# Performance work log

Measured on AMD Instinct MI355X. Metric: run time of the kernel, lower is better.

## Reference

```python
import jax, jax.numpy as jnp
import numpy as np

RANK = 8
ALPHA = 16.0
SCALING = ALPHA / RANK


def setup_inputs() -> dict:
    key = jax.random.key(0)
    ks = jax.random.split(key, 13)
    T, B, D = 8, 1024, 1024
    H1, H2, H3 = 2048, 2048, 1024
    r = RANK
    def n(k, shape, scale):
        return jax.random.normal(k, shape, dtype=jnp.float32) * scale
    return {
        "x": n(ks[0], (T, B, D), 1.0),
        "k0": n(ks[1], (D, H1), D ** -0.5),
        "b0": n(ks[2], (H1,), 0.02),
        "d0": n(ks[3], (D, r, T), D ** -0.5),
        "u0": n(ks[4], (r, H1, T), 0.02),  # zeros-init in original; random for nontrivial test
        "k1": n(ks[5], (H1, H2), H1 ** -0.5),
        "b1": n(ks[6], (H2,), 0.02),
        "d1": n(ks[7], (H1, r, T), H1 ** -0.5),
        "u1": n(ks[8], (r, H2, T), 0.02),
        "k2": n(ks[9], (H2, H3), H2 ** -0.5),
        "b2": n(ks[10], (H3,), 0.02),
        "d2": n(ks[11], (H2, r, T), H2 ** -0.5),
        "u2": n(ks[12], (r, H3, T), 0.02),
    }


def _lora_dense(h, k, b, d, u):
    # frozen base matmul: [t,b,i] @ [i,f] -> [t,b,f]
    base = jnp.einsum('tbi,if->tbf', h, k) + b
    # per-task low-rank adapter: down [i,r,t], up [r,f,t]
    delta = jnp.einsum('tbi,irt,rft->tbf', h, d, u) * SCALING
    return base + delta


def reference(x, k0, b0, d0, u0, k1, b1, d1, u1, k2, b2, d2, u2):
    h = jax.nn.relu(_lora_dense(x, k0, b0, d0, u0))
    h = jax.nn.relu(_lora_dense(h, k1, b1, d1, u1))
    h = _lora_dense(h, k2, b2, d2, u2)  # no activation on final layer
    return h
```

## Files before the change

### kernel.cpp

```cpp
#include <hip/hip_runtime.h>

typedef unsigned short u16;
typedef __attribute__((ext_vector_type(8))) __bf16 bf16x8;
typedef __attribute__((ext_vector_type(8))) unsigned short u16x8;
typedef __attribute__((ext_vector_type(4))) unsigned short u16x4;
typedef __attribute__((ext_vector_type(4))) float f32x4;

__device__ __forceinline__ float bf2f(u16 h) {
    return __uint_as_float(((unsigned int)h) << 16);
}
__device__ __forceinline__ u16 f2bf(float f) {
    unsigned int u = __float_as_uint(f);
    u += 0x7fffu + ((u >> 16) & 1u);
    return (u16)(u >> 16);
}
__device__ __forceinline__ bf16x8 zero_bf16x8() {
    union { unsigned int u[4]; bf16x8 v; } z;
    z.u[0] = z.u[1] = z.u[2] = z.u[3] = 0u;
    return z.v;
}
__device__ __forceinline__ void gload_lds16(const void* g, void* l) {
    __builtin_amdgcn_global_load_lds(
        (const __attribute__((address_space(1))) unsigned int*)g,
        (__attribute__((address_space(3))) unsigned int*)l, 16, 0, 0);
}
__device__ __forceinline__ void store_out(u16* p, float v)  { *p = f2bf(v); }
__device__ __forceinline__ void store_out(float* p, float v){ *p = v; }


__device__ __forceinline__ void do_cvt(
    const float* __restrict__ in, u16* __restrict__ out, int blk)
{
    int i = (blk * 256 + (int)threadIdx.x) * 8;
    float4 a = *(const float4*)(in + i);
    float4 b = *(const float4*)(in + i + 4);
    u16x8 o;
    o[0] = f2bf(a.x); o[1] = f2bf(a.y); o[2] = f2bf(a.z); o[3] = f2bf(a.w);
    o[4] = f2bf(b.x); o[5] = f2bf(b.y); o[6] = f2bf(b.z); o[7] = f2bf(b.w);
    *(u16x8*)(out + i) = o;
}

__device__ __forceinline__ void do_transpose64(
    const float* __restrict__ in, u16* __restrict__ out, int K, int F, int t)
{
    __shared__ u16 tt[64][68];
    int fb = t % (F >> 6), kb = t / (F >> 6);
    int f0 = fb << 6, k0 = kb << 6;
    int c  = threadIdx.x & 15;
    int r  = threadIdx.x >> 4;
#pragma unroll
    for (int p = 0; p < 4; ++p) {
        int row = p * 16 + r;
        float4 v = *(const float4*)(in + (size_t)(k0 + row) * F + f0 + c * 4);
        u16x4 w;
        w[0] = f2bf(v.x); w[1] = f2bf(v.y); w[2] = f2bf(v.z); w[3] = f2bf(v.w);
        *(u16x4*)&tt[row][c * 4] = w;
    }
    __syncthreads();
#pragma unroll
    for (int p = 0; p < 4; ++p) {
        int f = p * 16 + r;
        u16x4 w;
        w[0] = tt[c * 4 + 0][f];
        w[1] = tt[c * 4 + 1][f];
        w[2] = tt[c * 4 + 2][f];
        w[3] = tt[c * 4 + 3][f];
        *(u16x4*)(out + (size_t)(f0 + f) * K + k0 + c * 4) = w;
    }
}

__device__ __forceinline__ void do_prep_d(
    const float* __restrict__ d, u16* __restrict__ o, int K, int blk)
{
    int i = blk * 256 + (int)threadIdx.x;
    int r = i & 7;
    int k = (i >> 3) % K;
    int t = i / (K * 8);
    o[i] = f2bf(d[((size_t)k * 8 + r) * 8 + t]);
}

__device__ __forceinline__ void do_prep_u(
    const float* __restrict__ u, u16* __restrict__ o, int F, int blk)
{
    int i = blk * 256 + (int)threadIdx.x;
    int r = i & 7;
    int f = (i >> 3) % F;
    int t = i / (F * 8);
    o[i] = f2bf(u[((size_t)r * F + f) * 8 + t] * 2.0f);
}

__global__ __launch_bounds__(256) void prep_all(
    const float* x, const float* k0, const float* k1, const float* k2,
    const float* d0, const float* d1, const float* d2,
    const float* u0, const float* u1, const float* u2,
    u16* xb, u16* k0T, u16* k1T, u16* k2T,
    u16* dS0, u16* dS1, u16* dS2, u16* uS0, u16* uS1, u16* uS2)
{
    int b = blockIdx.x;
    if      (b < 4096) do_cvt(x, xb, b);
    else if (b < 4608) do_transpose64(k0, k0T, 1024, 2048, b - 4096);
    else if (b < 5632) do_transpose64(k1, k1T, 2048, 2048, b - 4608);
    else if (b < 6144) do_transpose64(k2, k2T, 2048, 1024, b - 5632);
    else if (b < 6400) do_prep_d(d0, dS0, 1024, b - 6144);
    else if (b < 6912) do_prep_d(d1, dS1, 2048, b - 6400);
    else if (b < 7424) do_prep_d(d2, dS2, 2048, b - 6912);
    else if (b < 7936) do_prep_u(u0, uS0, 2048, b - 7424);
    else if (b < 8448) do_prep_u(u1, uS1, 2048, b - 7936);
    else               do_prep_u(u2, uS2, 1024, b - 8448);
}

__global__ __launch_bounds__(256) void lora_down(
    const u16* __restrict__ H, const u16* __restrict__ dS,
    u16* __restrict__ Aout, int K)
{
    int gt   = blockIdx.x * 256 + threadIdx.x;
    int row  = gt >> 3;
    int oct  = gt & 7;
    int task = row >> 10;
    const u16* hrow = H  + (size_t)row * K;
    const u16* dt   = dS + (size_t)task * K * 8;
    float acc[8];
#pragma unroll
    for (int r = 0; r < 8; ++r) acc[r] = 0.f;
    int kpt  = K >> 3;
    int kbeg = oct * kpt;
    for (int kk = kbeg; kk < kbeg + kpt; kk += 8) {
        u16x8 h8 = *(const u16x8*)(hrow + kk);
#pragma unroll
        for (int j = 0; j < 8; ++j) {
            float hv = bf2f(h8[j]);
            u16x8 dv = *(const u16x8*)(dt + (size_t)(kk + j) * 8);
#pragma unroll
            for (int r = 0; r < 8; ++r)
                acc[r] += hv * bf2f(dv[r]);
        }
    }
#pragma unroll
    for (int r = 0; r < 8; ++r) {
        acc[r] += __shfl_xor(acc[r], 1);
        acc[r] += __shfl_xor(acc[r], 2);
        acc[r] += __shfl_xor(acc[r], 4);
    }
    if (oct == 0) {
        u16x8 o;
#pragma unroll
        for (int r = 0; r < 8; ++r) o[r] = f2bf(acc[r]);
        *(u16x8*)(Aout + (size_t)row * 8) = o;
    }
}


#define WVMC do { if constexpr (SAL + SBL == 4) { \
                    asm volatile("s_waitcnt vmcnt(4)" ::: "memory"); \
                  } else if constexpr (SAL + SBL == 3) { \
                    asm volatile("s_waitcnt vmcnt(3)" ::: "memory"); \
                  } else { \
                    asm volatile("s_waitcnt vmcnt(2)" ::: "memory"); } } while (0)
#define WVMP do { if constexpr (SAL == 2) { \
                    asm volatile("s_waitcnt vmcnt(2)" ::: "memory"); \
                  } else { \
                    asm volatile("s_waitcnt vmcnt(1)" ::: "memory"); } } while (0)
#define WVM0  asm volatile("s_waitcnt vmcnt(0)" ::: "memory")
#define PHASE_END do { __builtin_amdgcn_sched_barrier(0); \
                       __builtin_amdgcn_s_barrier(); } while (0)

#define DS_A(c, mh) do { \
    _Pragma("unroll") for (int mm = 0; mm < NMH; ++mm) \
    _Pragma("unroll") for (int ks = 0; ks < 2; ++ks) \
        aF[mm][ks] = *(const bf16x8*)((const char*)&sA[c][0] + \
                       arowb + ((mh)*NMH+mm)*4096 + (ks ? cb1 : cb0)); } while (0)

#define DS_B(c, nh, bset) do { \
    _Pragma("unroll") for (int nn = 0; nn < NBH; ++nn) \
    _Pragma("unroll") for (int ks = 0; ks < 2; ++ks) \
        bset[nn][ks] = *(const bf16x8*)((const char*)&sB[c][0] + \
                       browb + ((nh)*NBH+nn)*8192 + (ks ? cb1 : cb0)); } while (0)

#define MFMAQ(mh, nh, bset) do { \
    _Pragma("unroll") for (int ks = 0; ks < 2; ++ks) \
    _Pragma("unroll") for (int mm = 0; mm < NMH; ++mm) \
    _Pragma("unroll") for (int nn = 0; nn < NBH; ++nn) \
        acc[(mh)*NMH+mm][(nh)*NBH+nn] = __builtin_amdgcn_mfma_f32_16x16x32_bf16( \
            aF[mm][ks], bset[nn][ks], acc[(mh)*NMH+mm][(nh)*NBH+nn], 0, 0, 0); } while (0)

#define STAGE_A(c, h, kt) do { \
    _Pragma("unroll") for (int s = 0; s < SAL; ++s) \
        gload_lds16((const char*)A + (size_t)(unsigned)(aBase + \
                      ((h)*BMH + s*64)*(K*2) + (kt)*128), \
                    (char*)&sA[c][0] + (h)*(BMH*128) + s*8192 + tdst); } while (0)

#define STAGE_B(c, h, kt) do { \
    _Pragma("unroll") for (int s = 0; s < SBL; ++s) \
        gload_lds16((const char*)BT + (size_t)(unsigned)(bBase + \
                      ((h)*BNH + s*64)*(K*2) + (kt)*128), \
                    (char*)&sB[c][0] + (h)*(BNH*128) + s*8192 + tdst); } while (0)

template<int RELU, int BM, int BN, int WPEU, typename OUT_T>
__global__ __launch_bounds__(512, WPEU) void gemm_lora8(
    const u16* __restrict__ A, const u16* __restrict__ BT,
    const u16* __restrict__ ALR, const u16* __restrict__ US,
    const float* __restrict__ bias, OUT_T* __restrict__ C,
    int N, int K)
{
    constexpr int SAL = BM / 128;
    constexpr int SBL = BN / 128;
    constexpr int NMH = BM / 64;
    constexpr int NMB = BM / 32;
    constexpr int NBH = BN / 128;
    constexpr int NBN = BN / 64;
    constexpr int BMH = BM / 2;
    constexpr int BNH = BN / 2;

    __shared__ __align__(16) u16 sA[2][BM * 64];
    __shared__ __align__(16) u16 sB[2][BN * 64];

    const int tid  = threadIdx.x;
    const int lane = tid & 63;
    const int wave = tid >> 6;
    const int wr   = wave >> 2;
    const int wc   = wave & 3;
    const int l15  = lane & 15;
    const int lg   = lane >> 4;

    const int nwg = gridDim.x;
    const int orig = blockIdx.x;
    const int q = nwg >> 3, r = nwg & 7;
    const int x = orig & 7, o = orig >> 3;
    const int wg = (x < r ? x * (q + 1) : r * (q + 1) + (x - r) * q) + o;
    const int nbn  = N / BN;
    const int bm   = wg / nbn;
    const int bn   = wg % nbn;
    const int brow = bm * BM;
    const int bcol = bn * BN;
    const int task = brow >> 10;

    const int trow = tid >> 3;
    const int tkc  = (tid & 7) ^ (trow & 7);
    const int tdst = tid * 16;
    const int aBase = (brow + trow) * (K * 2) + tkc * 16;
    const int bBase = (bcol + trow) * (K * 2) + tkc * 16;

    const int rp    = l15 & 7;
    const int cb0   = ((lg ^ (rp & 3)) << 4) | ((rp & 4) << 4);
    const int cb1   = cb0 ^ 64;
    const int arowb = (wr * 16 + l15) * 128;
    const int browb = (wc * 16 + l15) * 128;

    f32x4 acc[NMB][NBN];
    const f32x4 zf = {0.f, 0.f, 0.f, 0.f};
#pragma unroll
    for (int m = 0; m < NMB; ++m)
#pragma unroll
        for (int n = 0; n < NBN; ++n) acc[m][n] = zf;

    bf16x8 aF[NMH][2], bF0[NBH][2], bF1[NBH][2];

    STAGE_A(0, 0, 0); STAGE_B(0, 0, 0); STAGE_A(0, 1, 0); STAGE_B(0, 1, 0);
    STAGE_A(1, 0, 1); STAGE_B(1, 0, 1);
    WVMC;
    PHASE_END;
    DS_A(0, 0); DS_B(0, 0, bF0);

    const int iters = K >> 7;
#pragma unroll 1
    for (int i = 0; i < iters; ++i) {
        const int t1 = 2 * i + 1, t2 = 2 * i + 2, t3 = 2 * i + 3;
        const bool nl = (i + 1 < iters);

        STAGE_A(1, 1, t1);
        MFMAQ(0, 0, bF0);
        DS_B(0, 1, bF1);
        PHASE_END;
        STAGE_B(1, 1, t1);
        MFMAQ(0, 1, bF1);
        DS_A(0, 1);
        PHASE_END;
        if (nl) STAGE_A(0, 0, t2);
        MFMAQ(1, 0, bF0);
        if (nl) { WVMP; } else { WVM0; }
        PHASE_END;
        if (nl) STAGE_B(0, 0, t2);
        MFMAQ(1, 1, bF1);
        DS_A(1, 0); DS_B(1, 0, bF0);
        PHASE_END;
        if (nl) STAGE_A(0, 1, t2);
        MFMAQ(0, 0, bF0);
        DS_B(1, 1, bF1);
        PHASE_END;
        if (nl) STAGE_B(0, 1, t2);
        MFMAQ(0, 1, bF1);
        DS_A(1, 1);
        PHASE_END;
        if (nl) STAGE_A(1, 0, t3);
        MFMAQ(1, 0, bF0);
        if (nl) { WVMP; }
        PHASE_END;
        if (nl) STAGE_B(1, 0, t3);
        MFMAQ(1, 1, bF1);
        if (nl) { DS_A(0, 0); DS_B(0, 0, bF0); }
        PHASE_END;
    }

    bf16x8 z8 = zero_bf16x8();
    bf16x8 bU[NBN];
#pragma unroll
    for (int n = 0; n < NBN; ++n) {
        int col = bcol + n * 64 + wc * 16 + l15;
        bU[n] = (lg == 0) ? *(const bf16x8*)(US + ((size_t)task * N + col) * 8) : z8;
    }
#pragma unroll
    for (int m = 0; m < NMB; ++m) {
        int row = brow + m * 32 + wr * 16 + l15;
        bf16x8 aL = (lg == 0) ? *(const bf16x8*)(ALR + (size_t)row * 8) : z8;
#pragma unroll
        for (int n = 0; n < NBN; ++n)
            acc[m][n] = __builtin_amdgcn_mfma_f32_16x16x32_bf16(
                aL, bU[n], acc[m][n], 0, 0, 0);
    }

#pragma unroll
    for (int n = 0; n < NBN; ++n) {
        int col  = bcol + n * 64 + wc * 16 + l15;
        float bv = bias[col];
#pragma unroll
        for (int m = 0; m < NMB; ++m) {
            int row0 = brow + m * 32 + wr * 16 + lg * 4;
#pragma unroll
            for (int rr = 0; rr < 4; ++rr) {
                float v = acc[m][n][rr] + bv;
                if (RELU) v = fmaxf(v, 0.0f);
                store_out(&C[(size_t)(row0 + rr) * N + col], v);
            }
        }
    }
}


extern "C" void kernel_launch(void* const* d_in, const int* in_sizes, int n_in,
                              void* d_out, int out_size, void* d_ws, size_t ws_size,
                              hipStream_t stream) {
    const float* x  = (const float*)d_in[0];
    const float* k0 = (const float*)d_in[1];
    const float* b0 = (const float*)d_in[2];
    const float* d0 = (const float*)d_in[3];
    const float* u0 = (const float*)d_in[4];
    const float* k1 = (const float*)d_in[5];
    const float* b1 = (const float*)d_in[6];
    const float* d1 = (const float*)d_in[7];
    const float* u1 = (const float*)d_in[8];
    const float* k2 = (const float*)d_in[9];
    const float* b2 = (const float*)d_in[10];
    const float* d2 = (const float*)d_in[11];
    const float* u2 = (const float*)d_in[12];

    const int T = 8, B = 1024, D = 1024, H1 = 2048, H2 = 2048, H3 = 1024;
    const int M = T * B;

    u16* w = (u16*)d_ws;
    size_t off = 0;
    u16* xb  = w + off; off += (size_t)M * D;
    u16* k0T = w + off; off += (size_t)H1 * D;
    u16* k1T = w + off; off += (size_t)H2 * H1;
    u16* k2T = w + off; off += (size_t)H3 * H2;
    u16* dS0 = w + off; off += (size_t)T * D * 8;
    u16* dS1 = w + off; off += (size_t)T * H1 * 8;
    u16* dS2 = w + off; off += (size_t)T * H2 * 8;
    u16* uS0 = w + off; off += (size_t)T * H1 * 8;
    u16* uS1 = w + off; off += (size_t)T * H2 * 8;
    u16* uS2 = w + off; off += (size_t)T * H3 * 8;
    u16* h1  = w + off; off += (size_t)M * H1;
    u16* h2  = w + off; off += (size_t)M * H2;
    u16* Ab  = w + off; off += (size_t)M * 8;
    (void)ws_size; (void)in_sizes; (void)n_in; (void)out_size;

    prep_all<<<8704, 256, 0, stream>>>(
        x, k0, k1, k2, d0, d1, d2, u0, u1, u2,
        xb, k0T, k1T, k2T, dS0, dS1, dS2, uS0, uS1, uS2);

    lora_down<<<(M * 8) / 256, 256, 0, stream>>>(xb, dS0, Ab, D);
    gemm_lora8<1, 256, 256, 2, u16><<<(M / 256) * (H1 / 256), 512, 0, stream>>>(
        xb, k0T, Ab, uS0, b0, h1, H1, D);
    lora_down<<<(M * 8) / 256, 256, 0, stream>>>(h1, dS1, Ab, H1);
    gemm_lora8<1, 256, 256, 2, u16><<<(M / 256) * (H2 / 256), 512, 0, stream>>>(
        h1, k1T, Ab, uS1, b1, h2, H2, H1);
    lora_down<<<(M * 8) / 256, 256, 0, stream>>>(h2, dS2, Ab, H2);
    gemm_lora8<0, 128, 128, 4, float><<<(M / 128) * (H3 / 128), 512, 0, stream>>>(
        h2, k2T, Ab, uS2, b2, (float*)d_out, H3, H2);
}
```

Baseline: 258.4 us.

## Fuse next layer's LoRA down-projection into GEMM epilogue via per-column-block partial sums

Each GEMM epilogue now multiplies its activated output tile by the next layer's down-projection weights, reduces across lanes and waves through LDS, and writes fp32 partial rank-8 sums per column block. The next GEMM sums those 8 slices and converts them to bf16 for the adapter MFMA. This removes two standalone lora_down kernels, which each re-read the full h1/h2 activations. In exchange it adds epilogue shuffle/LDS work, an extra barrier, partial-sum buffers in the workspace, and a small numerical change because the down-projection now uses fp32 activations rather than bf16-rounded ones.

```diff
diff --git a/kernel.cpp b/kernel.cpp
--- a/kernel.cpp
+++ b/kernel.cpp
@@ -14,10 +14,10 @@
     u += 0x7fffu + ((u >> 16) & 1u);
     return (u16)(u >> 16);
 }
+union bfu { u16x8 u; bf16x8 b; };
 __device__ __forceinline__ bf16x8 zero_bf16x8() {
-    union { unsigned int u[4]; bf16x8 v; } z;
-    z.u[0] = z.u[1] = z.u[2] = z.u[3] = 0u;
-    return z.v;
+    bfu z; z.u[0]=0;z.u[1]=0;z.u[2]=0;z.u[3]=0;z.u[4]=0;z.u[5]=0;z.u[6]=0;z.u[7]=0;
+    return z.b;
 }
 __device__ __forceinline__ void gload_lds16(const void* g, void* l) {
     __builtin_amdgcn_global_load_lds(
@@ -195,11 +195,12 @@
                       ((h)*BNH + s*64)*(K*2) + (kt)*128), \
                     (char*)&sB[c][0] + (h)*(BNH*128) + s*8192 + tdst); } while (0)
 
-template<int RELU, int BM, int BN, int WPEU, typename OUT_T>
+template<int RELU, int BM, int BN, int WPEU, int FSLICE, int FUSE, typename OUT_T>
 __global__ __launch_bounds__(512, WPEU) void gemm_lora8(
     const u16* __restrict__ A, const u16* __restrict__ BT,
-    const u16* __restrict__ ALR, const u16* __restrict__ US,
+    const void* __restrict__ ALR, const u16* __restrict__ US,
     const float* __restrict__ bias, OUT_T* __restrict__ C,
+    const u16* __restrict__ DSN, float* __restrict__ ABOUT,
     int N, int K)
 {
     constexpr int SAL = BM / 128;
@@ -311,25 +312,90 @@
 #pragma unroll
     for (int m = 0; m < NMB; ++m) {
         int row = brow + m * 32 + wr * 16 + l15;
-        bf16x8 aL = (lg == 0) ? *(const bf16x8*)(ALR + (size_t)row * 8) : z8;
+        bf16x8 aL;
+        if (lg == 0) {
+            if constexpr (FSLICE == 0) {
+                aL = *(const bf16x8*)((const u16*)ALR + (size_t)row * 8);
+            } else {
+                f32x4 lo = zf, hi = zf;
+#pragma unroll
+                for (int s = 0; s < FSLICE; ++s) {
+                    const float* sp = (const float*)ALR + (size_t)s * 8192 * 8
+                                      + (size_t)row * 8;
+                    lo += *(const f32x4*)sp;
+                    hi += *(const f32x4*)(sp + 4);
+                }
+                bfu t;
+#pragma unroll
+                for (int j = 0; j < 4; ++j) { t.u[j] = f2bf(lo[j]); t.u[4+j] = f2bf(hi[j]); }
+                aL = t.b;
+            }
+        } else aL = z8;
 #pragma unroll
         for (int n = 0; n < NBN; ++n)
             acc[m][n] = __builtin_amdgcn_mfma_f32_16x16x32_bf16(
                 aL, bU[n], acc[m][n], 0, 0, 0);
     }
 
-#pragma unroll
-    for (int n = 0; n < NBN; ++n) {
-        int col  = bcol + n * 64 + wc * 16 + l15;
-        float bv = bias[col];
+    if constexpr (FUSE) {
+        float dSf[NBN][8];
+#pragma unroll
+        for (int n = 0; n < NBN; ++n) {
+            int col = bcol + n * 64 + wc * 16 + l15;
+            u16x8 dv = *(const u16x8*)(DSN + ((size_t)task * N + col) * 8);
+#pragma unroll
+            for (int rr = 0; rr < 8; ++rr) dSf[n][rr] = bf2f(dv[rr]);
+        }
+        float* ldsP = (float*)&sA[0][0];
 #pragma unroll
         for (int m = 0; m < NMB; ++m) {
-            int row0 = brow + m * 32 + wr * 16 + lg * 4;
 #pragma unroll
             for (int rr = 0; rr < 4; ++rr) {
-                float v = acc[m][n][rr] + bv;
-                if (RELU) v = fmaxf(v, 0.0f);
-                store_out(&C[(size_t)(row0 + rr) * N + col], v);
+                int rl  = m * 32 + wr * 16 + lg * 4 + rr;
+                int row = brow + rl;
+                float p[8];
+#pragma unroll
+                for (int j = 0; j < 8; ++j) p[j] = 0.f;
+#pragma unroll
+                for (int n = 0; n < NBN; ++n) {
+                    int col  = bcol + n * 64 + wc * 16 + l15;
+                    float v = acc[m][n][rr] + bias[col];
+                    if (RELU) v = fmaxf(v, 0.0f);
+                    store_out(&C[(size_t)row * N + col], v);
+#pragma unroll
+                    for (int j = 0; j < 8; ++j) p[j] += v * dSf[n][j];
+                }
+#pragma unroll
+                for (int s = 1; s < 16; s <<= 1)
+#pragma unroll
+                    for (int j = 0; j < 8; ++j) p[j] += __shfl_xor(p[j], s);
+                if (l15 == 0) {
+                    f32x4 w0 = {p[0], p[1], p[2], p[3]};
+                    f32x4 w1 = {p[4], p[5], p[6], p[7]};
+                    *(f32x4*)&ldsP[(wc * 256 + rl) * 8]     = w0;
+                    *(f32x4*)&ldsP[(wc * 256 + rl) * 8 + 4] = w1;
+                }
+            }
+        }
+        __syncthreads();
+        for (int i = tid; i < 2048; i += 512) {
+            float s = ldsP[i] + ldsP[2048 + i] + ldsP[4096 + i] + ldsP[6144 + i];
+            ABOUT[(size_t)bn * (8192 * 8) + (size_t)brow * 8 + i] = s;
+        }
+    } else {
+#pragma unroll
+        for (int n = 0; n < NBN; ++n) {
+            int col  = bcol + n * 64 + wc * 16 + l15;
+            float bv = bias[col];
+#pragma unroll
+            for (int m = 0; m < NMB; ++m) {
+                int row0 = brow + m * 32 + wr * 16 + lg * 4;
+#pragma unroll
+                for (int rr = 0; rr < 4; ++rr) {
+                    float v = acc[m][n][rr] + bv;
+                    if (RELU) v = fmaxf(v, 0.0f);
+                    store_out(&C[(size_t)(row0 + rr) * N + col], v);
+                }
             }
         }
     }
@@ -371,6 +437,8 @@
     u16* h1  = w + off; off += (size_t)M * H1;
     u16* h2  = w + off; off += (size_t)M * H2;
     u16* Ab  = w + off; off += (size_t)M * 8;
+    float* AbP1 = (float*)(w + off); off += (size_t)8 * M * 8 * 2;
+    float* AbP2 = (float*)(w + off); off += (size_t)8 * M * 8 * 2;
     (void)ws_size; (void)in_sizes; (void)n_in; (void)out_size;
 
     prep_all<<<8704, 256, 0, stream>>>(
@@ -378,12 +446,14 @@
         xb, k0T, k1T, k2T, dS0, dS1, dS2, uS0, uS1, uS2);
 
     lora_down<<<(M * 8) / 256, 256, 0, stream>>>(xb, dS0, Ab, D);
-    gemm_lora8<1, 256, 256, 2, u16><<<(M / 256) * (H1 / 256), 512, 0, stream>>>(
-        xb, k0T, Ab, uS0, b0, h1, H1, D);
-    lora_down<<<(M * 8) / 256, 256, 0, stream>>>(h1, dS1, Ab, H1);
-    gemm_lora8<1, 256, 256, 2, u16><<<(M / 256) * (H2 / 256), 512, 0, stream>>>(
-        h1, k1T, Ab, uS1, b1, h2, H2, H1);
-    lora_down<<<(M * 8) / 256, 256, 0, stream>>>(h2, dS2, Ab, H2);
-    gemm_lora8<0, 128, 128, 4, float><<<(M / 128) * (H3 / 128), 512, 0, stream>>>(
-        h2, k2T, Ab, uS2, b2, (float*)d_out, H3, H2);
-}
+    gemm_lora8<1, 256, 256, 2, 0, 1, u16>
+        <<<(M / 256) * (H1 / 256), 512, 0, stream>>>(
+        xb, k0T, Ab, uS0, b0, h1, dS1, AbP1, H1, D);
+    gemm_lora8<1, 256, 256, 2, 8, 1, u16>
+        <<<(M / 256) * (H2 / 256), 512, 0, stream>>>(
+        h1, k1T, AbP1, uS1, b1, h2, dS2, AbP2, H2, H1);
+    gemm_lora8<0, 128, 128, 4, 8, 0, float>
+        <<<(M / 128) * (H3 / 128), 512, 0, stream>>>(
+        h2, k2T, AbP2, uS2, b2, (float*)d_out, (const u16*)nullptr,
+        (float*)nullptr, H3, H2);
+}
```

Measured after the change: 270.6 us. 1.05x slower.
